# Optimization experiments

Measured on AMD Instinct MI355X. Metric: run time of the kernel, lower is better.

## Reference

```python
import jax, jax.numpy as jnp
import numpy as np

B, N, T = 8192, 100, 64  # batch, ROI nodes, BOLD timepoints/features
GCN_DIMS = [(T, 32), (32, 16), (16, 8), (8, 4), (4, 2)]
EPS = 1e-5


def _kaiming(key, fout, fin):
    return jax.random.normal(key, (fout, fin), jnp.float32) * np.float32(np.sqrt(2.0 / fin))


def setup_inputs() -> dict:
    key = jax.random.key(0)
    ks = jax.random.split(key, 10)
    inp = {"BOLD_signals": jax.random.normal(ks[0], (B, N, T), jnp.float32)}
    inp["Wq"] = _kaiming(ks[1], 32, 64); inp["bq"] = jnp.zeros((32,), jnp.float32)
    inp["Wk"] = _kaiming(ks[2], 32, 64); inp["bk"] = jnp.zeros((32,), jnp.float32)
    inp["Wv"] = _kaiming(ks[3], 32, 64); inp["bv"] = jnp.zeros((32,), jnp.float32)
    for i, (fin, fout) in enumerate(GCN_DIMS):
        inp[f"W{i+1}"] = _kaiming(ks[4 + i], fout, fin)
        inp[f"b{i+1}"] = jnp.zeros((fout,), jnp.float32)
    inp["Wf"] = _kaiming(ks[9], 2, 200); inp["bf"] = jnp.zeros((2,), jnp.float32)
    return inp


def _corrcoef_batched(feat):
    # feat: [B, N, D]; rows are variables -> [B, N, N] correlation (torch.corrcoef, clipped)
    xc = feat - feat.mean(axis=-1, keepdims=True)
    cov = jnp.einsum('bnd,bmd->bnm', xc, xc)  # unnormalized; divisor cancels
    d = jnp.sqrt(jnp.einsum('bnn->bn', cov))
    corr = cov / (d[:, :, None] * d[:, None, :])
    return jnp.clip(corr, -1.0, 1.0)


def _batchnorm_nodes(h):
    # BatchNorm1d(100) on [B, 100, C]: normalize per node over (batch, feature) dims;
    # gamma=1, beta=0 per the module's constant init; training-mode batch stats.
    mean = h.mean(axis=(0, 2), keepdims=True)
    var = ((h - mean) ** 2).mean(axis=(0, 2), keepdims=True)
    return (h - mean) * jax.lax.rsqrt(var + EPS)


def _gcn(corr, h, W, b):
    z = jnp.einsum('bnm,bmf->bnf', corr, h) @ W.T + b
    return jnp.tanh(_batchnorm_nodes(z))


def reference(BOLD_signals, Wq, bq, Wk, bk, Wv, bv,
              W1, b1, W2, b2, W3, b3, W4, b4, W5, b5, Wf, bf):
    x = BOLD_signals
    Q = x @ Wq.T + bq
    K = x @ Wk.T + bk
    V = x @ Wv.T + bv
    A = jax.nn.softmax(jnp.einsum('bnd,bmd->bnm', Q, K) / 32.0, axis=2)
    feat = jnp.einsum('bnm,bmd->bnd', A, V)  # [B, N, 32]
    corr = _corrcoef_batched(feat)           # [B, N, N]
    h = x
    for (W, b) in [(W1, b1), (W2, b2), (W3, b3), (W4, b4), (W5, b5)]:
        h = _gcn(corr, h, W, b)
    out = h.reshape(h.shape[0], -1) @ Wf.T + bf  # [B, 2]
    return out
```

## Files before the change

kernel.cpp:

```cpp
#include <hip/hip_runtime.h>
#include <hip/hip_bf16.h>


typedef unsigned int u32;

__device__ __forceinline__ float blo(u32 u) { return __uint_as_float(u << 16); }
__device__ __forceinline__ float bhi(u32 u) { return __uint_as_float(u & 0xffff0000u); }

#define OFF_V  41600
#define OFF_Q  48400
#define OFF_K  55200
#define OFF_FE 48400
#define OFF_T0 62000
#define SMEM_KA 75200

__global__ __launch_bounds__(256, 2) void ka_kernel(
    const float* __restrict__ x,
    const float* __restrict__ Wq, const float* __restrict__ bq,
    const float* __restrict__ Wk, const float* __restrict__ bk,
    const float* __restrict__ Wv, const float* __restrict__ bv,
    const float* __restrict__ W1, const float* __restrict__ b1,
    __hip_bfloat16* __restrict__ corr_g,
    float* __restrict__ z1g,
    float* __restrict__ stats1)
{
  __shared__ __align__(16) char smem[SMEM_KA];
  const int b   = blockIdx.x;
  const int tid = threadIdx.x;

  {
    float4* xs4 = (float4*)smem;
    const float4* xg4 = (const float4*)(x + (size_t)b * 6400);
    for (int i4 = tid; i4 < 1600; i4 += 256) {
      int n = i4 >> 4, t4 = i4 & 15;
      xs4[n * 17 + t4] = xg4[i4];
    }
  }
  __syncthreads();

  {
    const int j = tid & 31, g = tid >> 5;
    float aq[13], ak[13], av[13], at[13];
#pragma unroll
    for (int k = 0; k < 13; ++k) { aq[k] = 0.f; ak[k] = 0.f; av[k] = 0.f; at[k] = 0.f; }
    const float4* Wq4 = (const float4*)Wq;
    const float4* Wk4 = (const float4*)Wk;
    const float4* Wv4 = (const float4*)Wv;
    const float4* W14 = (const float4*)W1;
    const float4* xs4 = (const float4*)smem;
#pragma unroll 4
    for (int t4 = 0; t4 < 16; ++t4) {
      float4 wqv = Wq4[(j << 4) | t4];
      float4 wkv = Wk4[(j << 4) | t4];
      float4 wvv = Wv4[(j << 4) | t4];
      float4 w1v = W14[(j << 4) | t4];
#pragma unroll
      for (int k = 0; k < 13; ++k) {
        float4 xv = xs4[(g + (k << 3)) * 17 + t4];
        aq[k] = fmaf(xv.x, wqv.x, fmaf(xv.y, wqv.y, fmaf(xv.z, wqv.z, fmaf(xv.w, wqv.w, aq[k]))));
        ak[k] = fmaf(xv.x, wkv.x, fmaf(xv.y, wkv.y, fmaf(xv.z, wkv.z, fmaf(xv.w, wkv.w, ak[k]))));
        av[k] = fmaf(xv.x, wvv.x, fmaf(xv.y, wvv.y, fmaf(xv.z, wvv.z, fmaf(xv.w, wvv.w, av[k]))));
        at[k] = fmaf(xv.x, w1v.x, fmaf(xv.y, w1v.y, fmaf(xv.z, w1v.z, fmaf(xv.w, w1v.w, at[k]))));
      }
    }
    __hip_bfloat16* Qb = (__hip_bfloat16*)(smem + OFF_Q);
    __hip_bfloat16* Kb = (__hip_bfloat16*)(smem + OFF_K);
    __hip_bfloat16* Vb = (__hip_bfloat16*)(smem + OFF_V);
    float* t0 = (float*)(smem + OFF_T0);
    float bqj = bq[j], bkj = bk[j], bvj = bv[j];
#pragma unroll
    for (int k = 0; k < 13; ++k) {
      int n = g + (k << 3);
      if (n < 100) {
        Qb[n * 34 + j] = __float2bfloat16(aq[k] + bqj);
        Kb[n * 34 + j] = __float2bfloat16(ak[k] + bkj);
        Vb[n * 34 + j] = __float2bfloat16(av[k] + bvj);
        t0[n * 33 + j] = at[k];
      }
    }
  }
  __syncthreads();

  {
    const int lane = tid & 63, wvid = tid >> 6;
    float s0a[25], s1a[25];
#pragma unroll
    for (int r = 0; r < 25; ++r) { s0a[r] = 0.f; s1a[r] = 0.f; }
    const u32* Qu  = (const u32*)(smem + OFF_Q);
    const u32* Ku0 = (const u32*)(smem + OFF_K) + lane * 17;
    const u32* Ku1 = Ku0 + 64 * 17;
#pragma unroll 4
    for (int t2 = 0; t2 < 16; ++t2) {
      u32 k0 = Ku0[t2], k1 = Ku1[t2];
      float k0l = blo(k0), k0h = bhi(k0), k1l = blo(k1), k1h = bhi(k1);
#pragma unroll
      for (int r = 0; r < 25; ++r) {
        u32 qu = Qu[(wvid + (r << 2)) * 17 + t2];
        float ql = blo(qu), qh = bhi(qu);
        s0a[r] = fmaf(ql, k0l, fmaf(qh, k0h, s0a[r]));
        s1a[r] = fmaf(ql, k1l, fmaf(qh, k1h, s1a[r]));
      }
    }
    const bool m1ok = lane < 36;
    float* A = (float*)smem;
#pragma unroll
    for (int r = 0; r < 25; ++r) {
      int n = wvid + (r << 2);
      float s0 = s0a[r];
      float s1 = m1ok ? s1a[r] : -3.0e38f;
      float sm = fmaxf(s0, s1);
#pragma unroll
      for (int off = 32; off; off >>= 1) sm = fmaxf(sm, __shfl_xor(sm, off, 64));
      float e0 = __expf((s0 - sm) * 0.03125f);
      float e1 = m1ok ? __expf((s1 - sm) * 0.03125f) : 0.f;
      float sum = e0 + e1;
#pragma unroll
      for (int off = 32; off; off >>= 1) sum += __shfl_xor(sum, off, 64);
      float rr = 1.0f / sum;
      A[n * 104 + lane] = e0 * rr;
      if (m1ok) A[n * 104 + 64 + lane] = e1 * rr;
    }
  }
  __syncthreads();

  {
    const int j = tid & 31, g = tid >> 5;
    float fa[13];
#pragma unroll
    for (int k = 0; k < 13; ++k) fa[k] = 0.f;
    const float4* A4 = (const float4*)smem;
    const __hip_bfloat16* Vb = (const __hip_bfloat16*)(smem + OFF_V);
#pragma unroll 5
    for (int m4 = 0; m4 < 25; ++m4) {
      float v0 = __bfloat162float(Vb[(m4 * 4 + 0) * 34 + j]);
      float v1 = __bfloat162float(Vb[(m4 * 4 + 1) * 34 + j]);
      float v2 = __bfloat162float(Vb[(m4 * 4 + 2) * 34 + j]);
      float v3 = __bfloat162float(Vb[(m4 * 4 + 3) * 34 + j]);
#pragma unroll
      for (int k = 0; k < 13; ++k) {
        float4 a = A4[(g + (k << 3)) * 26 + m4];
        fa[k] = fmaf(a.x, v0, fmaf(a.y, v1, fmaf(a.z, v2, fmaf(a.w, v3, fa[k]))));
      }
    }
    float* featL = (float*)(smem + OFF_FE);
#pragma unroll
    for (int k = 0; k < 13; ++k) {
      int n = g + (k << 3);
      float v = fa[k];
      float rs = v;
#pragma unroll
      for (int off = 16; off; off >>= 1) rs += __shfl_xor(rs, off, 32);
      float xc = v - rs * 0.03125f;
      float s2 = xc * xc;
#pragma unroll
      for (int off = 16; off; off >>= 1) s2 += __shfl_xor(s2, off, 32);
      float inv = rsqrtf(s2);
      if (n < 100) featL[n * 33 + j] = xc * inv;
    }
  }
  __syncthreads();

  {
    const int lane = tid & 63, wvid = tid >> 6;
    float c0a[25], c1a[25];
#pragma unroll
    for (int r = 0; r < 25; ++r) { c0a[r] = 0.f; c1a[r] = 0.f; }
    const float* featL = (const float*)(smem + OFF_FE);
    const float* ca = featL + lane * 33;
    const float* cb = featL + (lane + 64) * 33;
#pragma unroll 4
    for (int t = 0; t < 32; ++t) {
      float a = ca[t], bb = cb[t];
#pragma unroll
      for (int r = 0; r < 25; ++r) {
        float q = featL[(wvid + (r << 2)) * 33 + t];
        c0a[r] = fmaf(q, a, c0a[r]);
        c1a[r] = fmaf(q, bb, c1a[r]);
      }
    }
    float* corrL = (float*)smem;
    __hip_bfloat16* cg = corr_g + (size_t)b * 10000;
    const bool mok = lane < 36;
#pragma unroll
    for (int r = 0; r < 25; ++r) {
      int n = wvid + (r << 2);
      float d0 = fminf(1.f, fmaxf(-1.f, c0a[r]));
      corrL[n * 104 + lane] = d0;
      cg[n * 100 + lane] = __float2bfloat16(d0);
      if (mok) {
        float d1 = fminf(1.f, fmaxf(-1.f, c1a[r]));
        corrL[n * 104 + 64 + lane] = d1;
        cg[n * 100 + 64 + lane] = __float2bfloat16(d1);
      }
    }
  }
  __syncthreads();

  {
    const int j = tid & 31, g = tid >> 5;
    float acc[13];
    float bj = b1[j];
#pragma unroll
    for (int k = 0; k < 13; ++k) acc[k] = bj;
    const float4* c4 = (const float4*)smem;
    const float* t0 = (const float*)(smem + OFF_T0);
#pragma unroll 5
    for (int m4 = 0; m4 < 25; ++m4) {
      float ta = t0[(m4 * 4 + 0) * 33 + j];
      float tb = t0[(m4 * 4 + 1) * 33 + j];
      float tc = t0[(m4 * 4 + 2) * 33 + j];
      float td = t0[(m4 * 4 + 3) * 33 + j];
#pragma unroll
      for (int k = 0; k < 13; ++k) {
        float4 c = c4[(g + (k << 3)) * 26 + m4];
        acc[k] = fmaf(c.x, ta, fmaf(c.y, tb, fmaf(c.z, tc, fmaf(c.w, td, acc[k]))));
      }
    }
    float* zo = z1g + (size_t)b * 3200;
#pragma unroll
    for (int k = 0; k < 13; ++k) {
      int n = g + (k << 3);
      if (n < 100) {
        float v = acc[k];
        zo[n * 32 + j] = v;
        float s = v, ss = v * v;
#pragma unroll
        for (int off = 16; off; off >>= 1) {
          s  += __shfl_xor(s, off, 32);
          ss += __shfl_xor(ss, off, 32);
        }
        if (j == 0) {
          atomicAdd(&stats1[n], s);
          atomicAdd(&stats1[100 + n], ss);
        }
      }
    }
  }
}

template<int FIN, int FOUT>
__global__ __launch_bounds__(256, 2) void kb_kernel(
    const float* __restrict__ zin,
    const __hip_bfloat16* __restrict__ corr_g,
    const float* __restrict__ W, const float* __restrict__ bias,
    const float* __restrict__ stats_in, float* __restrict__ stats_out,
    float* __restrict__ zout)
{
  constexpr int LOGF  = (FOUT == 16) ? 4 : (FOUT == 8) ? 3 : (FOUT == 4) ? 2 : 1;
  constexpr int LOGFI = (FIN == 32) ? 5 : (FIN == 16) ? 4 : (FIN == 8) ? 3 : 2;
  constexpr int RP = 256 / FOUT;
  constexpr int NR = (100 + RP - 1) / RP;

  __shared__ float mS[100], vS[100];
  __shared__ float hL[100 * 33];
  __shared__ float tL[100 * (FOUT + 1)];
  __shared__ __align__(16) float clL[100 * 104];

  const int b = blockIdx.x, tid = threadIdx.x;

  {
    const u32* cgu = (const u32*)(corr_g + (size_t)b * 10000);
    for (int u = tid; u < 5000; u += 256) {
      int n = (u * 5243) >> 18;
      int mm = (u - n * 50) << 1;
      u32 cc = cgu[u];
      clL[n * 104 + mm]     = blo(cc);
      clL[n * 104 + mm + 1] = bhi(cc);
    }
  }
  if (tid < 100) {
    float cnt  = 8192.0f * (float)FIN;
    float mean = stats_in[tid] / cnt;
    float var  = stats_in[100 + tid] / cnt - mean * mean;
    mS[tid] = mean;
    vS[tid] = rsqrtf(var + 1e-5f);
  }
  __syncthreads();

  {
    const float4* zb4 = (const float4*)(zin + (size_t)b * 100 * FIN);
    for (int i4 = tid; i4 < 25 * FIN; i4 += 256) {
      int n = i4 >> (LOGFI - 2);
      int c = (i4 << 2) & (FIN - 1);
      float4 z = zb4[i4];
      float mn = mS[n], iv = vS[n];
      hL[n * 33 + c + 0] = tanhf((z.x - mn) * iv);
      hL[n * 33 + c + 1] = tanhf((z.y - mn) * iv);
      hL[n * 33 + c + 2] = tanhf((z.z - mn) * iv);
      hL[n * 33 + c + 3] = tanhf((z.w - mn) * iv);
    }
  }
  __syncthreads();

  const int j  = tid & (FOUT - 1);
  const int nb = tid >> LOGF;

  {
    float wreg[FIN];
#pragma unroll
    for (int c = 0; c < FIN; ++c) wreg[c] = W[j * FIN + c];
#pragma unroll
    for (int k = 0; k < NR; ++k) {
      int n = nb + k * RP;
      if (n < 100) {
        float a = 0.f;
#pragma unroll
        for (int c = 0; c < FIN; ++c) a = fmaf(hL[n * 33 + c], wreg[c], a);
        tL[n * (FOUT + 1) + j] = a;
      }
    }
  }
  __syncthreads();

  {
    float acc[NR];
    float bj = bias[j];
#pragma unroll
    for (int k = 0; k < NR; ++k) acc[k] = bj;
    int nrow[NR];
#pragma unroll
    for (int k = 0; k < NR; ++k) nrow[k] = min(nb + k * RP, 99);
    const float4* c4 = (const float4*)clL;
#pragma unroll 5
    for (int m4 = 0; m4 < 25; ++m4) {
      float ta = tL[(m4 * 4 + 0) * (FOUT + 1) + j];
      float tb = tL[(m4 * 4 + 1) * (FOUT + 1) + j];
      float tc = tL[(m4 * 4 + 2) * (FOUT + 1) + j];
      float td = tL[(m4 * 4 + 3) * (FOUT + 1) + j];
#pragma unroll
      for (int k = 0; k < NR; ++k) {
        float4 c = c4[nrow[k] * 26 + m4];
        acc[k] = fmaf(c.x, ta, fmaf(c.y, tb, fmaf(c.z, tc, fmaf(c.w, td, acc[k]))));
      }
    }
    float* zo = zout + (size_t)b * 100 * FOUT;
#pragma unroll
    for (int k = 0; k < NR; ++k) {
      int n = nb + k * RP;
      if (n < 100) {
        float v = acc[k];
        zo[n * FOUT + j] = v;
        float s = v, ss = v * v;
#pragma unroll
        for (int off = FOUT >> 1; off; off >>= 1) {
          s  += __shfl_xor(s, off, FOUT);
          ss += __shfl_xor(ss, off, FOUT);
        }
        if (j == 0) {
          atomicAdd(&stats_out[n], s);
          atomicAdd(&stats_out[100 + n], ss);
        }
      }
    }
  }
}

__global__ __launch_bounds__(256) void kf_kernel(
    const float* __restrict__ z5, const float* __restrict__ stats5,
    const float* __restrict__ Wf, const float* __restrict__ bfv,
    float* __restrict__ out)
{
  __shared__ float mS[100], vS[100];
  const int tid = threadIdx.x;
  if (tid < 100) {
    float cnt  = 8192.0f * 2.0f;
    float mean = stats5[tid] / cnt;
    float var  = stats5[100 + tid] / cnt - mean * mean;
    mS[tid] = mean;
    vS[tid] = rsqrtf(var + 1e-5f);
  }
  __syncthreads();
  const int wvid = tid >> 6, lane = tid & 63;
  const int b = blockIdx.x * 4 + wvid;
  const float* zb = z5 + (size_t)b * 200;
  float a0 = 0.f, a1 = 0.f;
#pragma unroll
  for (int p = 0; p < 4; ++p) {
    int jj = lane + p * 64;
    if (jj < 200) {
      int n = jj >> 1;
      float hv = tanhf((zb[jj] - mS[n]) * vS[n]);
      a0 = fmaf(hv, Wf[jj], a0);
      a1 = fmaf(hv, Wf[200 + jj], a1);
    }
  }
#pragma unroll
  for (int off = 32; off; off >>= 1) {
    a0 += __shfl_xor(a0, off, 64);
    a1 += __shfl_xor(a1, off, 64);
  }
  if (lane == 0) {
    out[b * 2 + 0] = a0 + bfv[0];
    out[b * 2 + 1] = a1 + bfv[1];
  }
}

extern "C" void kernel_launch(void* const* d_in, const int* in_sizes, int n_in,
                              void* d_out, int out_size, void* d_ws, size_t ws_size,
                              hipStream_t stream)
{
  const float* x  = (const float*)d_in[0];
  const float* Wq = (const float*)d_in[1];
  const float* bq = (const float*)d_in[2];
  const float* Wk = (const float*)d_in[3];
  const float* bk = (const float*)d_in[4];
  const float* Wv = (const float*)d_in[5];
  const float* bv = (const float*)d_in[6];
  const float* W1 = (const float*)d_in[7];
  const float* b1 = (const float*)d_in[8];
  const float* W2 = (const float*)d_in[9];
  const float* b2 = (const float*)d_in[10];
  const float* W3 = (const float*)d_in[11];
  const float* b3 = (const float*)d_in[12];
  const float* W4 = (const float*)d_in[13];
  const float* b4 = (const float*)d_in[14];
  const float* W5 = (const float*)d_in[15];
  const float* b5 = (const float*)d_in[16];
  const float* Wf = (const float*)d_in[17];
  const float* bf = (const float*)d_in[18];
  float* out = (float*)d_out;

  char* ws = (char*)d_ws;
  const size_t NEED = 321130400ull;
  if (ws_size < NEED) return;

  __hip_bfloat16* corr_g = (__hip_bfloat16*)ws;
  float* zA    = (float*)(ws + 163840000ull);
  float* zB    = (float*)(ws + 268697600ull);
  float* stats = (float*)(ws + 321126400ull);

  hipMemsetAsync(stats, 0, 5 * 200 * sizeof(float), stream);

  ka_kernel<<<8192, 256, 0, stream>>>(x, Wq, bq, Wk, bk, Wv, bv, W1, b1,
                                      corr_g, zA, stats);
  kb_kernel<32, 16><<<8192, 256, 0, stream>>>(zA, corr_g, W2, b2, stats,       stats + 200, zB);
  kb_kernel<16,  8><<<8192, 256, 0, stream>>>(zB, corr_g, W3, b3, stats + 200, stats + 400, zA);
  kb_kernel< 8,  4><<<8192, 256, 0, stream>>>(zA, corr_g, W4, b4, stats + 400, stats + 600, zB);
  kb_kernel< 4,  2><<<8192, 256, 0, stream>>>(zB, corr_g, W5, b5, stats + 600, stats + 800, zA);
  kf_kernel<<<2048, 256, 0, stream>>>(zA, stats + 800, Wf, bf, out);
}
```

Baseline: 4.339 ms.

## Move attention, correlation and GCN matmuls onto bf16 MFMA with hi/lo split

Replaces the scalar FMA matmuls in the attention/correlation kernel and the GCN layer kernels with 16x16x32 bf16 MFMA instructions. To keep accuracy close to fp32, operands are split into bf16 high and low parts and combined across several MFMAs. The kernel goes to 512 threads, shared-memory layouts are reorganised into padded bf16 tiles, and tanhf is swapped for an exp-based approximation. The risks are some precision loss from the bf16 split and the fast tanh, higher shared-memory use per block, and idle waves in the 7-tile stages.

```diff
diff --git a/kernel.cpp b/kernel.cpp
--- a/kernel.cpp
+++ b/kernel.cpp
@@ -3,18 +3,46 @@
 
 
 typedef unsigned int u32;
-
-__device__ __forceinline__ float blo(u32 u) { return __uint_as_float(u << 16); }
-__device__ __forceinline__ float bhi(u32 u) { return __uint_as_float(u & 0xffff0000u); }
-
-#define OFF_V  41600
-#define OFF_Q  48400
-#define OFF_K  55200
-#define OFF_FE 48400
-#define OFF_T0 62000
-#define SMEM_KA 75200
-
-__global__ __launch_bounds__(256, 2) void ka_kernel(
+typedef unsigned short u16;
+typedef float f32x4 __attribute__((ext_vector_type(4)));
+typedef short s16x8 __attribute__((ext_vector_type(8)));
+
+__device__ __forceinline__ f32x4 mfma16(s16x8 a, s16x8 b, f32x4 c) {
+  return __builtin_amdgcn_mfma_f32_16x16x32_bf16(a, b, c, 0, 0, 0);
+}
+__device__ __forceinline__ u16 f2b(float f) {
+  __hip_bfloat16 h = __float2bfloat16(f);
+  u16 u; __builtin_memcpy(&u, &h, 2); return u;
+}
+__device__ __forceinline__ float b2f(u16 u) { return __uint_as_float((u32)u << 16); }
+__device__ __forceinline__ u32 pack_hi2(float a, float b) { return (u32)f2b(a) | ((u32)f2b(b) << 16); }
+__device__ __forceinline__ u32 pack_lo2(float a, float b) {
+  return (u32)f2b(a - b2f(f2b(a))) | ((u32)f2b(b - b2f(f2b(b))) << 16);
+}
+__device__ __forceinline__ float fast_tanh(float x) {
+  float e = __expf(2.0f * x);
+  return 1.0f - 2.0f * __builtin_amdgcn_rcpf(e + 1.0f);
+}
+
+#define KA_XHI   0
+#define KA_XLO   8064
+#define KA_WHI   16128
+#define KA_WLO   25344
+#define KA_AHI   0
+#define KA_ALO   15232
+#define KA_CHI   0
+#define KA_CLO   15232
+#define KA_Q     34560
+#define KA_K     39040
+#define KA_VT    43520
+#define KA_T0H   47872
+#define KA_T0L   52224
+#define KA_SX    72
+#define KA_ASX   136
+#define KA_QSX   40
+#define KA_SMEM  113152
+
+__global__ __launch_bounds__(512, 2) void ka_kernel(
     const float* __restrict__ x,
     const float* __restrict__ Wq, const float* __restrict__ bq,
     const float* __restrict__ Wk, const float* __restrict__ bk,
@@ -24,222 +52,222 @@
     float* __restrict__ z1g,
     float* __restrict__ stats1)
 {
-  __shared__ __align__(16) char smem[SMEM_KA];
-  const int b   = blockIdx.x;
-  const int tid = threadIdx.x;
-
-  {
-    float4* xs4 = (float4*)smem;
-    const float4* xg4 = (const float4*)(x + (size_t)b * 6400);
-    for (int i4 = tid; i4 < 1600; i4 += 256) {
-      int n = i4 >> 4, t4 = i4 & 15;
-      xs4[n * 17 + t4] = xg4[i4];
-    }
-  }
-  __syncthreads();
-
-  {
-    const int j = tid & 31, g = tid >> 5;
-    float aq[13], ak[13], av[13], at[13];
-#pragma unroll
-    for (int k = 0; k < 13; ++k) { aq[k] = 0.f; ak[k] = 0.f; av[k] = 0.f; at[k] = 0.f; }
-    const float4* Wq4 = (const float4*)Wq;
-    const float4* Wk4 = (const float4*)Wk;
-    const float4* Wv4 = (const float4*)Wv;
-    const float4* W14 = (const float4*)W1;
-    const float4* xs4 = (const float4*)smem;
-#pragma unroll 4
-    for (int t4 = 0; t4 < 16; ++t4) {
-      float4 wqv = Wq4[(j << 4) | t4];
-      float4 wkv = Wk4[(j << 4) | t4];
-      float4 wvv = Wv4[(j << 4) | t4];
-      float4 w1v = W14[(j << 4) | t4];
-#pragma unroll
-      for (int k = 0; k < 13; ++k) {
-        float4 xv = xs4[(g + (k << 3)) * 17 + t4];
-        aq[k] = fmaf(xv.x, wqv.x, fmaf(xv.y, wqv.y, fmaf(xv.z, wqv.z, fmaf(xv.w, wqv.w, aq[k]))));
-        ak[k] = fmaf(xv.x, wkv.x, fmaf(xv.y, wkv.y, fmaf(xv.z, wkv.z, fmaf(xv.w, wkv.w, ak[k]))));
-        av[k] = fmaf(xv.x, wvv.x, fmaf(xv.y, wvv.y, fmaf(xv.z, wvv.z, fmaf(xv.w, wvv.w, av[k]))));
-        at[k] = fmaf(xv.x, w1v.x, fmaf(xv.y, w1v.y, fmaf(xv.z, w1v.z, fmaf(xv.w, w1v.w, at[k]))));
-      }
-    }
-    __hip_bfloat16* Qb = (__hip_bfloat16*)(smem + OFF_Q);
-    __hip_bfloat16* Kb = (__hip_bfloat16*)(smem + OFF_K);
-    __hip_bfloat16* Vb = (__hip_bfloat16*)(smem + OFF_V);
-    float* t0 = (float*)(smem + OFF_T0);
-    float bqj = bq[j], bkj = bk[j], bvj = bv[j];
-#pragma unroll
-    for (int k = 0; k < 13; ++k) {
-      int n = g + (k << 3);
-      if (n < 100) {
-        Qb[n * 34 + j] = __float2bfloat16(aq[k] + bqj);
-        Kb[n * 34 + j] = __float2bfloat16(ak[k] + bkj);
-        Vb[n * 34 + j] = __float2bfloat16(av[k] + bvj);
-        t0[n * 33 + j] = at[k];
-      }
-    }
-  }
-  __syncthreads();
-
-  {
-    const int lane = tid & 63, wvid = tid >> 6;
-    float s0a[25], s1a[25];
-#pragma unroll
-    for (int r = 0; r < 25; ++r) { s0a[r] = 0.f; s1a[r] = 0.f; }
-    const u32* Qu  = (const u32*)(smem + OFF_Q);
-    const u32* Ku0 = (const u32*)(smem + OFF_K) + lane * 17;
-    const u32* Ku1 = Ku0 + 64 * 17;
-#pragma unroll 4
-    for (int t2 = 0; t2 < 16; ++t2) {
-      u32 k0 = Ku0[t2], k1 = Ku1[t2];
-      float k0l = blo(k0), k0h = bhi(k0), k1l = blo(k1), k1h = bhi(k1);
-#pragma unroll
-      for (int r = 0; r < 25; ++r) {
-        u32 qu = Qu[(wvid + (r << 2)) * 17 + t2];
-        float ql = blo(qu), qh = bhi(qu);
-        s0a[r] = fmaf(ql, k0l, fmaf(qh, k0h, s0a[r]));
-        s1a[r] = fmaf(ql, k1l, fmaf(qh, k1h, s1a[r]));
-      }
-    }
-    const bool m1ok = lane < 36;
-    float* A = (float*)smem;
-#pragma unroll
-    for (int r = 0; r < 25; ++r) {
-      int n = wvid + (r << 2);
-      float s0 = s0a[r];
-      float s1 = m1ok ? s1a[r] : -3.0e38f;
-      float sm = fmaxf(s0, s1);
-#pragma unroll
-      for (int off = 32; off; off >>= 1) sm = fmaxf(sm, __shfl_xor(sm, off, 64));
-      float e0 = __expf((s0 - sm) * 0.03125f);
-      float e1 = m1ok ? __expf((s1 - sm) * 0.03125f) : 0.f;
-      float sum = e0 + e1;
-#pragma unroll
-      for (int off = 32; off; off >>= 1) sum += __shfl_xor(sum, off, 64);
-      float rr = 1.0f / sum;
-      A[n * 104 + lane] = e0 * rr;
-      if (m1ok) A[n * 104 + 64 + lane] = e1 * rr;
-    }
-  }
-  __syncthreads();
-
-  {
-    const int j = tid & 31, g = tid >> 5;
-    float fa[13];
-#pragma unroll
-    for (int k = 0; k < 13; ++k) fa[k] = 0.f;
-    const float4* A4 = (const float4*)smem;
-    const __hip_bfloat16* Vb = (const __hip_bfloat16*)(smem + OFF_V);
-#pragma unroll 5
-    for (int m4 = 0; m4 < 25; ++m4) {
-      float v0 = __bfloat162float(Vb[(m4 * 4 + 0) * 34 + j]);
-      float v1 = __bfloat162float(Vb[(m4 * 4 + 1) * 34 + j]);
-      float v2 = __bfloat162float(Vb[(m4 * 4 + 2) * 34 + j]);
-      float v3 = __bfloat162float(Vb[(m4 * 4 + 3) * 34 + j]);
-#pragma unroll
-      for (int k = 0; k < 13; ++k) {
-        float4 a = A4[(g + (k << 3)) * 26 + m4];
-        fa[k] = fmaf(a.x, v0, fmaf(a.y, v1, fmaf(a.z, v2, fmaf(a.w, v3, fa[k]))));
-      }
-    }
-    float* featL = (float*)(smem + OFF_FE);
-#pragma unroll
-    for (int k = 0; k < 13; ++k) {
-      int n = g + (k << 3);
-      float v = fa[k];
-      float rs = v;
-#pragma unroll
-      for (int off = 16; off; off >>= 1) rs += __shfl_xor(rs, off, 32);
-      float xc = v - rs * 0.03125f;
-      float s2 = xc * xc;
-#pragma unroll
-      for (int off = 16; off; off >>= 1) s2 += __shfl_xor(s2, off, 32);
-      float inv = rsqrtf(s2);
-      if (n < 100) featL[n * 33 + j] = xc * inv;
-    }
-  }
-  __syncthreads();
-
-  {
-    const int lane = tid & 63, wvid = tid >> 6;
-    float c0a[25], c1a[25];
-#pragma unroll
-    for (int r = 0; r < 25; ++r) { c0a[r] = 0.f; c1a[r] = 0.f; }
-    const float* featL = (const float*)(smem + OFF_FE);
-    const float* ca = featL + lane * 33;
-    const float* cb = featL + (lane + 64) * 33;
-#pragma unroll 4
-    for (int t = 0; t < 32; ++t) {
-      float a = ca[t], bb = cb[t];
-#pragma unroll
-      for (int r = 0; r < 25; ++r) {
-        float q = featL[(wvid + (r << 2)) * 33 + t];
-        c0a[r] = fmaf(q, a, c0a[r]);
-        c1a[r] = fmaf(q, bb, c1a[r]);
-      }
-    }
-    float* corrL = (float*)smem;
-    __hip_bfloat16* cg = corr_g + (size_t)b * 10000;
-    const bool mok = lane < 36;
-#pragma unroll
-    for (int r = 0; r < 25; ++r) {
-      int n = wvid + (r << 2);
-      float d0 = fminf(1.f, fmaxf(-1.f, c0a[r]));
-      corrL[n * 104 + lane] = d0;
-      cg[n * 100 + lane] = __float2bfloat16(d0);
-      if (mok) {
-        float d1 = fminf(1.f, fmaxf(-1.f, c1a[r]));
-        corrL[n * 104 + 64 + lane] = d1;
-        cg[n * 100 + 64 + lane] = __float2bfloat16(d1);
-      }
-    }
-  }
-  __syncthreads();
-
-  {
-    const int j = tid & 31, g = tid >> 5;
-    float acc[13];
-    float bj = b1[j];
-#pragma unroll
-    for (int k = 0; k < 13; ++k) acc[k] = bj;
-    const float4* c4 = (const float4*)smem;
-    const float* t0 = (const float*)(smem + OFF_T0);
-#pragma unroll 5
-    for (int m4 = 0; m4 < 25; ++m4) {
-      float ta = t0[(m4 * 4 + 0) * 33 + j];
-      float tb = t0[(m4 * 4 + 1) * 33 + j];
-      float tc = t0[(m4 * 4 + 2) * 33 + j];
-      float td = t0[(m4 * 4 + 3) * 33 + j];
-#pragma unroll
-      for (int k = 0; k < 13; ++k) {
-        float4 c = c4[(g + (k << 3)) * 26 + m4];
-        acc[k] = fmaf(c.x, ta, fmaf(c.y, tb, fmaf(c.z, tc, fmaf(c.w, td, acc[k]))));
-      }
-    }
+  __shared__ __align__(16) char smem[KA_SMEM];
+  u16* S16 = (u16*)smem;
+  const int b = blockIdx.x, tid = threadIdx.x;
+  const int w = tid >> 6, l = tid & 63, l15 = l & 15, g = l >> 4;
+  const f32x4 zero4 = {0.f, 0.f, 0.f, 0.f};
+
+  {
+    const float2* xg2 = (const float2*)(x + (size_t)b * 6400);
+    for (int i = tid; i < 112 * 32; i += 512) {
+      int r = i >> 5, c2 = i & 31;
+      float vx = 0.f, vy = 0.f;
+      if (r < 100) { float2 v = xg2[r * 32 + c2]; vx = v.x; vy = v.y; }
+      *(u32*)&S16[KA_XHI + r * KA_SX + c2 * 2] = pack_hi2(vx, vy);
+      *(u32*)&S16[KA_XLO + r * KA_SX + c2 * 2] = pack_lo2(vx, vy);
+    }
+    for (int i = tid; i < 128 * 32; i += 512) {
+      int r = i >> 5, c2 = i & 31;
+      const float* Wp = (r < 32) ? Wq : (r < 64) ? Wk : (r < 96) ? Wv : W1;
+      float2 v = ((const float2*)Wp)[(r & 31) * 32 + c2];
+      *(u32*)&S16[KA_WHI + r * KA_SX + c2 * 2] = pack_hi2(v.x, v.y);
+      *(u32*)&S16[KA_WLO + r * KA_SX + c2 * 2] = pack_lo2(v.x, v.y);
+    }
+    for (int i = tid; i < 1152; i += 512) {
+      int arr = i / 384, rem = i - arr * 384;
+      int r = rem / 12, c = rem - r * 12;
+      int base = (arr == 0) ? KA_VT : (arr == 1) ? KA_T0H : KA_T0L;
+      *(u32*)&S16[base + r * KA_ASX + 112 + c * 2] = 0;
+    }
+  }
+  __syncthreads();
+
+  {
+    const int mi = w >> 1;
+    const int j = 16 * (w & 1) + l15;
+    float bias = 0.f;
+    if (mi == 0) bias = bq[j]; else if (mi == 1) bias = bk[j]; else if (mi == 2) bias = bv[j];
+    for (int tm = 0; tm < 7; ++tm) {
+      f32x4 acc = zero4;
+#pragma unroll
+      for (int kt = 0; kt < 2; ++kt) {
+        s16x8 ah = *(const s16x8*)&S16[KA_XHI + (16 * tm + l15) * KA_SX + g * 8 + kt * 32];
+        s16x8 al = *(const s16x8*)&S16[KA_XLO + (16 * tm + l15) * KA_SX + g * 8 + kt * 32];
+        s16x8 bh = *(const s16x8*)&S16[KA_WHI + (16 * w + l15) * KA_SX + g * 8 + kt * 32];
+        s16x8 bl = *(const s16x8*)&S16[KA_WLO + (16 * w + l15) * KA_SX + g * 8 + kt * 32];
+        acc = mfma16(al, bh, acc);
+        acc = mfma16(ah, bl, acc);
+        acc = mfma16(ah, bh, acc);
+      }
+      const int row0 = 16 * tm + 4 * g;
+#pragma unroll
+      for (int r = 0; r < 4; ++r) {
+        int row = row0 + r;
+        float v = acc[r] + bias;
+        u16 hv = f2b(v);
+        if (mi == 0)      S16[KA_Q  + row * KA_QSX + j] = hv;
+        else if (mi == 1) S16[KA_K  + row * KA_QSX + j] = hv;
+        else if (mi == 2) S16[KA_VT + j * KA_ASX + row] = hv;
+        else {
+          S16[KA_T0H + j * KA_ASX + row] = hv;
+          S16[KA_T0L + j * KA_ASX + row] = f2b(v - b2f(hv));
+        }
+      }
+    }
+  }
+  __syncthreads();
+
+  {
+    for (int i = tid; i < 2688; i += 512) {
+      int arr = i / 1344, rem = i - arr * 1344;
+      int r = rem / 12, c = rem - r * 12;
+      *(u32*)&S16[(arr ? KA_ALO : KA_AHI) + r * KA_ASX + 112 + c * 2] = 0;
+    }
+    if (w < 7) {
+      const int tm = w;
+      s16x8 aq = *(const s16x8*)&S16[KA_Q + (16 * tm + l15) * KA_QSX + g * 8];
+      f32x4 sc[7];
+#pragma unroll
+      for (int tn = 0; tn < 7; ++tn) {
+        s16x8 bb = *(const s16x8*)&S16[KA_K + (16 * tn + l15) * KA_QSX + g * 8];
+        sc[tn] = mfma16(aq, bb, zero4);
+      }
+      const int row0 = 16 * tm + 4 * g;
+#pragma unroll
+      for (int r = 0; r < 4; ++r) {
+        const int row = row0 + r;
+        float v[7];
+#pragma unroll
+        for (int tn = 0; tn < 7; ++tn) v[tn] = sc[tn][r];
+        if (l15 >= 4) v[6] = -3.0e38f;
+        float m = v[0];
+#pragma unroll
+        for (int tn = 1; tn < 7; ++tn) m = fmaxf(m, v[tn]);
+#pragma unroll
+        for (int off = 1; off < 16; off <<= 1) m = fmaxf(m, __shfl_xor(m, off, 16));
+        float e[7], s = 0.f;
+#pragma unroll
+        for (int tn = 0; tn < 7; ++tn) { e[tn] = __expf((v[tn] - m) * 0.03125f); s += e[tn]; }
+#pragma unroll
+        for (int off = 1; off < 16; off <<= 1) s += __shfl_xor(s, off, 16);
+        float rr = __builtin_amdgcn_rcpf(s);
+        bool ok = row < 100;
+#pragma unroll
+        for (int tn = 0; tn < 7; ++tn) {
+          float a = ok ? e[tn] * rr : 0.f;
+          u16 ah = f2b(a);
+          S16[KA_AHI + row * KA_ASX + 16 * tn + l15] = ah;
+          S16[KA_ALO + row * KA_ASX + 16 * tn + l15] = f2b(a - b2f(ah));
+        }
+      }
+    }
+  }
+  __syncthreads();
+
+  if (w < 7) {
+    const int tm = w;
+    f32x4 f0 = zero4, f1 = zero4;
+#pragma unroll
+    for (int kt = 0; kt < 4; ++kt) {
+      s16x8 ah  = *(const s16x8*)&S16[KA_AHI + (16 * tm + l15) * KA_ASX + g * 8 + kt * 32];
+      s16x8 al  = *(const s16x8*)&S16[KA_ALO + (16 * tm + l15) * KA_ASX + g * 8 + kt * 32];
+      s16x8 b0  = *(const s16x8*)&S16[KA_VT + l15 * KA_ASX + g * 8 + kt * 32];
+      s16x8 b1v = *(const s16x8*)&S16[KA_VT + (16 + l15) * KA_ASX + g * 8 + kt * 32];
+      f0 = mfma16(al, b0, f0);  f0 = mfma16(ah, b0, f0);
+      f1 = mfma16(al, b1v, f1); f1 = mfma16(ah, b1v, f1);
+    }
+    const int row0 = 16 * tm + 4 * g;
+#pragma unroll
+    for (int r = 0; r < 4; ++r) {
+      float v0 = f0[r], v1 = f1[r];
+      float s = v0 + v1;
+#pragma unroll
+      for (int off = 1; off < 16; off <<= 1) s += __shfl_xor(s, off, 16);
+      float mean = s * 0.03125f;
+      float xc0 = v0 - mean, xc1 = v1 - mean;
+      float q = xc0 * xc0 + xc1 * xc1;
+#pragma unroll
+      for (int off = 1; off < 16; off <<= 1) q += __shfl_xor(q, off, 16);
+      float inv = rsqrtf(q + 1e-30f);
+      const int row = row0 + r;
+      float c0 = xc0 * inv, c1 = xc1 * inv;
+      u16 h0 = f2b(c0), h1 = f2b(c1);
+      S16[KA_Q + row * KA_QSX + l15]      = h0;
+      S16[KA_Q + row * KA_QSX + 16 + l15] = h1;
+      S16[KA_K + row * KA_QSX + l15]      = f2b(c0 - b2f(h0));
+      S16[KA_K + row * KA_QSX + 16 + l15] = f2b(c1 - b2f(h1));
+    }
+  }
+  __syncthreads();
+
+  if (w < 7) {
+    u16* cgu = (u16*)(corr_g + (size_t)b * 10000);
+    const int tm = w;
+    s16x8 ah = *(const s16x8*)&S16[KA_Q + (16 * tm + l15) * KA_QSX + g * 8];
+    s16x8 al = *(const s16x8*)&S16[KA_K + (16 * tm + l15) * KA_QSX + g * 8];
+    const int row0 = 16 * tm + 4 * g;
+#pragma unroll
+    for (int tn = 0; tn < 7; ++tn) {
+      s16x8 bh = *(const s16x8*)&S16[KA_Q + (16 * tn + l15) * KA_QSX + g * 8];
+      s16x8 bl = *(const s16x8*)&S16[KA_K + (16 * tn + l15) * KA_QSX + g * 8];
+      f32x4 c = mfma16(al, bh, zero4);
+      c = mfma16(ah, bl, c);
+      c = mfma16(ah, bh, c);
+      const int col = 16 * tn + l15;
+#pragma unroll
+      for (int r = 0; r < 4; ++r) {
+        float d = fminf(1.f, fmaxf(-1.f, c[r]));
+        u16 ch = f2b(d);
+        const int row = row0 + r;
+        S16[KA_CHI + row * KA_ASX + col] = ch;
+        S16[KA_CLO + row * KA_ASX + col] = f2b(d - b2f(ch));
+        if (row < 100 && col < 100) cgu[row * 100 + col] = ch;
+      }
+    }
+  }
+  __syncthreads();
+
+  if (w < 7) {
+    const int tm = w;
+    float bj0 = b1[l15], bj1 = b1[16 + l15];
     float* zo = z1g + (size_t)b * 3200;
-#pragma unroll
-    for (int k = 0; k < 13; ++k) {
-      int n = g + (k << 3);
-      if (n < 100) {
-        float v = acc[k];
-        zo[n * 32 + j] = v;
-        float s = v, ss = v * v;
-#pragma unroll
-        for (int off = 16; off; off >>= 1) {
-          s  += __shfl_xor(s, off, 32);
-          ss += __shfl_xor(ss, off, 32);
-        }
-        if (j == 0) {
-          atomicAdd(&stats1[n], s);
-          atomicAdd(&stats1[100 + n], ss);
-        }
-      }
-    }
-  }
-}
+    f32x4 z0 = zero4, z1v = zero4;
+#pragma unroll
+    for (int kt = 0; kt < 4; ++kt) {
+      s16x8 a_h = *(const s16x8*)&S16[KA_CHI + (16 * tm + l15) * KA_ASX + g * 8 + kt * 32];
+      s16x8 a_l = *(const s16x8*)&S16[KA_CLO + (16 * tm + l15) * KA_ASX + g * 8 + kt * 32];
+      s16x8 b0h = *(const s16x8*)&S16[KA_T0H + l15 * KA_ASX + g * 8 + kt * 32];
+      s16x8 b0l = *(const s16x8*)&S16[KA_T0L + l15 * KA_ASX + g * 8 + kt * 32];
+      s16x8 b1h = *(const s16x8*)&S16[KA_T0H + (16 + l15) * KA_ASX + g * 8 + kt * 32];
+      s16x8 b1l = *(const s16x8*)&S16[KA_T0L + (16 + l15) * KA_ASX + g * 8 + kt * 32];
+      z0 = mfma16(a_l, b0h, z0);  z0 = mfma16(a_h, b0l, z0);  z0 = mfma16(a_h, b0h, z0);
+      z1v = mfma16(a_l, b1h, z1v); z1v = mfma16(a_h, b1l, z1v); z1v = mfma16(a_h, b1h, z1v);
+    }
+    const int row0 = 16 * tm + 4 * g;
+#pragma unroll
+    for (int r = 0; r < 4; ++r) {
+      const int row = row0 + r;
+      float v0 = z0[r] + bj0, v1 = z1v[r] + bj1;
+      if (row < 100) { zo[row * 32 + l15] = v0; zo[row * 32 + 16 + l15] = v1; }
+      float s = v0 + v1, ss = v0 * v0 + v1 * v1;
+#pragma unroll
+      for (int off = 1; off < 16; off <<= 1) {
+        s += __shfl_xor(s, off, 16); ss += __shfl_xor(ss, off, 16);
+      }
+      if (row < 100 && l15 == 0) { atomicAdd(&stats1[row], s); atomicAdd(&stats1[100 + row], ss); }
+    }
+  }
+}
+
+#define KB_HL   30464
+#define KB_TT   43664
+#define KB_TTL  48016
+#define KB_MS   52368
+#define KB_SMEM 53168
 
 template<int FIN, int FOUT>
-__global__ __launch_bounds__(256, 2) void kb_kernel(
+__global__ __launch_bounds__(256, 3) void kb_kernel(
     const float* __restrict__ zin,
     const __hip_bfloat16* __restrict__ corr_g,
     const float* __restrict__ W, const float* __restrict__ bias,
@@ -251,29 +279,41 @@
   constexpr int RP = 256 / FOUT;
   constexpr int NR = (100 + RP - 1) / RP;
 
-  __shared__ float mS[100], vS[100];
-  __shared__ float hL[100 * 33];
-  __shared__ float tL[100 * (FOUT + 1)];
-  __shared__ __align__(16) float clL[100 * 104];
+  __shared__ __align__(16) char smem[KB_SMEM];
+  u16* S16 = (u16*)smem;
+  float* hL = (float*)(smem + KB_HL);
+  u16* tt  = (u16*)(smem + KB_TT);
+  u16* ttl = (u16*)(smem + KB_TTL);
+  float* mS = (float*)(smem + KB_MS);
+  float* vS = mS + 100;
 
   const int b = blockIdx.x, tid = threadIdx.x;
+  const f32x4 zero4 = {0.f, 0.f, 0.f, 0.f};
 
   {
     const u32* cgu = (const u32*)(corr_g + (size_t)b * 10000);
-    for (int u = tid; u < 5000; u += 256) {
-      int n = (u * 5243) >> 18;
-      int mm = (u - n * 50) << 1;
-      u32 cc = cgu[u];
-      clL[n * 104 + mm]     = blo(cc);
-      clL[n * 104 + mm + 1] = bhi(cc);
-    }
-  }
-  if (tid < 100) {
-    float cnt  = 8192.0f * (float)FIN;
-    float mean = stats_in[tid] / cnt;
-    float var  = stats_in[100 + tid] / cnt - mean * mean;
-    mS[tid] = mean;
-    vS[tid] = rsqrtf(var + 1e-5f);
+    u32* cl = (u32*)smem;
+    for (int i = tid; i < 5000; i += 256) {
+      int n = (i * 5243) >> 18;
+      int mm = i - n * 50;
+      cl[n * 68 + mm] = cgu[i];
+    }
+    for (int i = tid; i < 1800; i += 256) {
+      int n = i / 18, c = i - n * 18;
+      cl[n * 68 + 50 + c] = 0;
+    }
+    for (int i = tid; i < 816; i += 256) {
+      int n = i / 68, c = i - n * 68;
+      cl[(100 + n) * 68 + c] = 0;
+    }
+    u32* ttz = (u32*)tt;
+    for (int i = tid; i < 2176; i += 256) ttz[i] = 0;
+    if (tid < 100) {
+      float cnt  = 8192.0f * (float)FIN;
+      float mean = stats_in[tid] / cnt;
+      float var  = stats_in[100 + tid] / cnt - mean * mean;
+      mS[tid] = mean; vS[tid] = rsqrtf(var + 1e-5f);
+    }
   }
   __syncthreads();
 
@@ -284,72 +324,64 @@
       int c = (i4 << 2) & (FIN - 1);
       float4 z = zb4[i4];
       float mn = mS[n], iv = vS[n];
-      hL[n * 33 + c + 0] = tanhf((z.x - mn) * iv);
-      hL[n * 33 + c + 1] = tanhf((z.y - mn) * iv);
-      hL[n * 33 + c + 2] = tanhf((z.z - mn) * iv);
-      hL[n * 33 + c + 3] = tanhf((z.w - mn) * iv);
-    }
-  }
-  __syncthreads();
-
-  const int j  = tid & (FOUT - 1);
-  const int nb = tid >> LOGF;
-
-  {
+      hL[n * 33 + c + 0] = fast_tanh((z.x - mn) * iv);
+      hL[n * 33 + c + 1] = fast_tanh((z.y - mn) * iv);
+      hL[n * 33 + c + 2] = fast_tanh((z.z - mn) * iv);
+      hL[n * 33 + c + 3] = fast_tanh((z.w - mn) * iv);
+    }
+  }
+  __syncthreads();
+
+  {
+    const int j = tid & (FOUT - 1);
+    const int nbk = tid >> LOGF;
     float wreg[FIN];
 #pragma unroll
     for (int c = 0; c < FIN; ++c) wreg[c] = W[j * FIN + c];
 #pragma unroll
     for (int k = 0; k < NR; ++k) {
-      int n = nb + k * RP;
+      int n = nbk + k * RP;
       if (n < 100) {
         float a = 0.f;
 #pragma unroll
         for (int c = 0; c < FIN; ++c) a = fmaf(hL[n * 33 + c], wreg[c], a);
-        tL[n * (FOUT + 1) + j] = a;
-      }
-    }
-  }
-  __syncthreads();
-
-  {
-    float acc[NR];
-    float bj = bias[j];
-#pragma unroll
-    for (int k = 0; k < NR; ++k) acc[k] = bj;
-    int nrow[NR];
-#pragma unroll
-    for (int k = 0; k < NR; ++k) nrow[k] = min(nb + k * RP, 99);
-    const float4* c4 = (const float4*)clL;
-#pragma unroll 5
-    for (int m4 = 0; m4 < 25; ++m4) {
-      float ta = tL[(m4 * 4 + 0) * (FOUT + 1) + j];
-      float tb = tL[(m4 * 4 + 1) * (FOUT + 1) + j];
-      float tc = tL[(m4 * 4 + 2) * (FOUT + 1) + j];
-      float td = tL[(m4 * 4 + 3) * (FOUT + 1) + j];
-#pragma unroll
-      for (int k = 0; k < NR; ++k) {
-        float4 c = c4[nrow[k] * 26 + m4];
-        acc[k] = fmaf(c.x, ta, fmaf(c.y, tb, fmaf(c.z, tc, fmaf(c.w, td, acc[k]))));
-      }
-    }
+        u16 hh = f2b(a);
+        tt[j * 136 + n]  = hh;
+        ttl[j * 136 + n] = f2b(a - b2f(hh));
+      }
+    }
+  }
+  __syncthreads();
+
+  {
+    const int w = tid >> 6, l15 = tid & 15, g = (tid & 63) >> 4;
+    const int nb = (w < 3) ? 2 : 1;
+    float bj = (l15 < FOUT) ? bias[l15] : 0.f;
     float* zo = zout + (size_t)b * 100 * FOUT;
-#pragma unroll
-    for (int k = 0; k < NR; ++k) {
-      int n = nb + k * RP;
-      if (n < 100) {
-        float v = acc[k];
-        zo[n * FOUT + j] = v;
-        float s = v, ss = v * v;
-#pragma unroll
-        for (int off = FOUT >> 1; off; off >>= 1) {
-          s  += __shfl_xor(s, off, FOUT);
-          ss += __shfl_xor(ss, off, FOUT);
+    for (int bi = 0; bi < nb; ++bi) {
+      const int tm = w + 4 * bi;
+      f32x4 acc = zero4;
+#pragma unroll
+      for (int kt = 0; kt < 4; ++kt) {
+        s16x8 a  = *(const s16x8*)&S16[(16 * tm + l15) * 136 + g * 8 + kt * 32];
+        s16x8 bh = *(const s16x8*)&tt[l15 * 136 + g * 8 + kt * 32];
+        s16x8 bl = *(const s16x8*)&ttl[l15 * 136 + g * 8 + kt * 32];
+        acc = mfma16(a, bl, acc);
+        acc = mfma16(a, bh, acc);
+      }
+      const int row0 = 16 * tm + 4 * g;
+      const bool jok = l15 < FOUT;
+#pragma unroll
+      for (int r = 0; r < 4; ++r) {
+        const int row = row0 + r;
+        float v = acc[r] + bj;
+        if (row < 100 && jok) zo[row * FOUT + l15] = v;
+        float s = jok ? v : 0.f, ss = jok ? v * v : 0.f;
+#pragma unroll
+        for (int off = 1; off < 16; off <<= 1) {
+          s += __shfl_xor(s, off, 16); ss += __shfl_xor(ss, off, 16);
         }
-        if (j == 0) {
-          atomicAdd(&stats_out[n], s);
-          atomicAdd(&stats_out[100 + n], ss);
-        }
+        if (row < 100 && l15 == 0) { atomicAdd(&stats_out[row], s); atomicAdd(&stats_out[100 + row], ss); }
       }
     }
   }
@@ -379,7 +411,7 @@
     int jj = lane + p * 64;
     if (jj < 200) {
       int n = jj >> 1;
-      float hv = tanhf((zb[jj] - mS[n]) * vS[n]);
+      float hv = fast_tanh((zb[jj] - mS[n]) * vS[n]);
       a0 = fmaf(hv, Wf[jj], a0);
       a1 = fmaf(hv, Wf[200 + jj], a1);
     }
@@ -429,9 +461,9 @@
   float* zB    = (float*)(ws + 268697600ull);
   float* stats = (float*)(ws + 321126400ull);
 
-  hipMemsetAsync(stats, 0, 5 * 200 * sizeof(float), stream);
-
-  ka_kernel<<<8192, 256, 0, stream>>>(x, Wq, bq, Wk, bk, Wv, bv, W1, b1,
+  (void)hipMemsetAsync(stats, 0, 5 * 200 * sizeof(float), stream);
+
+  ka_kernel<<<8192, 512, 0, stream>>>(x, Wq, bq, Wk, bk, Wv, bv, W1, b1,
                                       corr_g, zA, stats);
   kb_kernel<32, 16><<<8192, 256, 0, stream>>>(zA, corr_g, W2, b2, stats,       stats + 200, zB);
   kb_kernel<16,  8><<<8192, 256, 0, stream>>>(zB, corr_g, W3, b3, stats + 200, stats + 400, zA);
```

Result: slower. 8.487 ms (+95.6%).
